# Optimization experiments

Measured on AMD Instinct MI355X. Metric: run time of the kernel, lower is better.

Reference implementation:

```python
import jax, jax.numpy as jnp
import numpy as np

# ---- model hyperparams (match init_kwargs / Mamba1 defaults) ----
SEQ_LEN, PRED_LEN, PATCH, STRIDE = 512, 96, 16, 16
D_MODEL, N_LAYER, N_VARS = 128, 2, 32
D_INNER, D_STATE, D_CONV, DT_RANK = 2 * D_MODEL, 16, 4, 8  # d_inner=2*d_model, dt_rank=ceil(d_model/16)
BATCH = 16
EPS = 1e-5


def setup_inputs() -> dict:
    key = jax.random.key(0)
    ks = jax.random.split(key, 20)
    s = 0.02
    inp = {
        'x_enc': jax.random.normal(ks[0], (BATCH, SEQ_LEN, N_VARS), jnp.float32),
        'x_mark_enc': jax.random.normal(ks[1], (BATCH, SEQ_LEN, 4), jnp.float32),
        'x_dec': jax.random.normal(ks[2], (BATCH, PRED_LEN, N_VARS), jnp.float32),
        'x_mark_dec': jax.random.normal(ks[3], (BATCH, PRED_LEN, 4), jnp.float32),
        # patch embedding: Linear(patch_len -> d_model, bias=False)
        'patch_w': jax.random.normal(ks[4], (D_MODEL, PATCH), jnp.float32) * s,
        # per-layer Mamba1 params, stacked on leading layer axis
        'norm_w': jnp.ones((N_LAYER, D_MODEL), jnp.float32),
        'in_proj_w': jax.random.normal(ks[5], (N_LAYER, 2 * D_INNER, D_MODEL), jnp.float32) * s,
        'conv_w': jax.random.normal(ks[6], (N_LAYER, D_INNER, D_CONV), jnp.float32) * s,
        'conv_b': jnp.zeros((N_LAYER, D_INNER), jnp.float32),
        'x_proj_w': jax.random.normal(ks[7], (N_LAYER, DT_RANK + 2 * D_STATE, D_INNER), jnp.float32) * s,
        'dt_proj_w': jax.random.normal(ks[8], (N_LAYER, D_INNER, DT_RANK), jnp.float32) * s,
        'dt_proj_b': jax.random.normal(ks[9], (N_LAYER, D_INNER), jnp.float32) * 0.1 - 4.0,  # softplus -> small dt
        'A_log': jnp.tile(jnp.log(jnp.arange(1, D_STATE + 1, dtype=jnp.float32))[None, None, :], (N_LAYER, D_INNER, 1)),
        'D_skip': jnp.ones((N_LAYER, D_INNER), jnp.float32),
        'out_proj_w': jax.random.normal(ks[10], (N_LAYER, D_MODEL, D_INNER), jnp.float32) * s,
        'final_norm_w': jnp.ones((D_MODEL,), jnp.float32),
        # head: Linear(d_model*seq_len//patch_len -> pred_len)
        'head_w': jax.random.normal(ks[11], (PRED_LEN, D_MODEL * SEQ_LEN // PATCH), jnp.float32) * s,
        'head_b': jnp.zeros((PRED_LEN,), jnp.float32),
    }
    return inp


def rmsnorm(x, w):
    return x * jax.lax.rsqrt(jnp.mean(x * x, axis=-1, keepdims=True) + EPS) * w


def selective_scan(u, dt, A, Bm, Cm, Dp):
    # u, dt: (B,L,Di); Bm, Cm: (B,L,N); A: (Di,N); Dp: (Di,)
    def step(h, inp):
        dt_t, B_t, C_t, u_t = inp  # (B,Di),(B,N),(B,N),(B,Di)
        dA = jnp.exp(dt_t[:, :, None] * A)                      # (B,Di,N)
        h = dA * h + dt_t[:, :, None] * B_t[:, None, :] * u_t[:, :, None]
        y = jnp.einsum('bdn,bn->bd', h, C_t)
        return h, y

    B_, L, Di = u.shape
    h0 = jnp.zeros((B_, Di, A.shape[1]), u.dtype)
    xs = (dt.transpose(1, 0, 2), Bm.transpose(1, 0, 2), Cm.transpose(1, 0, 2), u.transpose(1, 0, 2))
    _, ys = jax.lax.scan(step, h0, xs)
    return ys.transpose(1, 0, 2) + u * Dp  # skip connection D*u


def mamba_mixer(x, in_w, cw, cb, xp_w, dt_w, dt_b, A_log, Dp, out_w):
    # x: (B,L,d_model)
    xz = x @ in_w.T                                   # (B,L,2*Di)
    xs_, z = jnp.split(xz, 2, axis=-1)
    xc = xs_.transpose(0, 2, 1)                       # (B,Di,L)
    xc = jax.lax.conv_general_dilated(
        xc, cw[:, None, :], (1,), [(D_CONV - 1, 0)],  # causal depthwise conv
        dimension_numbers=('NCH', 'OIH', 'NCH'), feature_group_count=D_INNER)
    xc = jax.nn.silu(xc + cb[None, :, None])
    u = xc.transpose(0, 2, 1)                         # (B,L,Di)
    x_dbl = u @ xp_w.T                                # (B,L,dt_rank+2N)
    dt, Bm, Cm = jnp.split(x_dbl, [DT_RANK, DT_RANK + D_STATE], axis=-1)
    dt = jax.nn.softplus(dt @ dt_w.T + dt_b)          # (B,L,Di)
    A = -jnp.exp(A_log)                               # (Di,N)
    y = selective_scan(u, dt, A, Bm, Cm, Dp)
    y = y * jax.nn.silu(z)
    return y @ out_w.T


def reference(x_enc, x_mark_enc, x_dec, x_mark_dec, patch_w, norm_w, in_proj_w,
              conv_w, conv_b, x_proj_w, dt_proj_w, dt_proj_b, A_log, D_skip,
              out_proj_w, final_norm_w, head_w, head_b):
    b, _, c = x_enc.shape
    # instance norm over time (stats detached)
    means = jax.lax.stop_gradient(jnp.mean(x_enc, axis=1, keepdims=True))
    xe = x_enc - means
    stdev = jax.lax.stop_gradient(jnp.sqrt(jnp.var(xe, axis=1, keepdims=True) + EPS))
    xe = xe / stdev
    # patching: stride == patch_len so unfold == reshape
    xp = xe.transpose(0, 2, 1).reshape(b, c, SEQ_LEN // PATCH, PATCH)  # (b,c,l,patch)
    enc = jnp.einsum('bclp,dp->bcld', xp, patch_w).reshape(b, c * (SEQ_LEN // PATCH), D_MODEL)
    # Mamba encoder: pre-norm residual blocks + final norm
    x = enc
    for i in range(N_LAYER):
        h = rmsnorm(x, norm_w[i])
        x = x + mamba_mixer(h, in_proj_w[i], conv_w[i], conv_b[i], x_proj_w[i],
                            dt_proj_w[i], dt_proj_b[i], A_log[i], D_skip[i], out_proj_w[i])
    x = rmsnorm(x, final_norm_w)
    # prediction head: b (c l) d -> (b c) (l d) -> linear -> (b, pred, c)
    l = SEQ_LEN // PATCH
    xh = x.reshape(b, c, l * D_MODEL)
    out = xh @ head_w.T + head_b                      # (b,c,pred)
    dec_out = out.transpose(0, 2, 1)                  # (b,pred,c)
    dec_out = dec_out * stdev[:, :1, :] + means[:, :1, :]
    return dec_out
```

## Files before the change

kernel.cpp:

```cpp
#include <hip/hip_runtime.h>
#include <hip/hip_bf16.h>
#include <math.h>

#define BATCH   16
#define SEQL    512
#define NVARS   32
#define PATCHL  16
#define LTOK    32
#define DMODEL  128
#define NLAYER  2
#define DIN     256
#define DSTATE  16
#define DTRANK  8
#define DCONV   4
#define PRED    96
#define TOK     1024
#define NTOK    (BATCH*TOK)
#define EPSF    1e-5f
#define NCH     64
#define CHL     16

typedef __attribute__((ext_vector_type(8))) short bf16x8;
typedef __attribute__((ext_vector_type(4))) float f32x4;
typedef __hip_bfloat16 bf16;

__global__ __launch_bounds__(256) void k_cast(
    const float* __restrict__ a, const float* __restrict__ b,
    const float* __restrict__ c, const float* __restrict__ d,
    int na, int nb, int nc, int nd, bf16* __restrict__ out,
    const float* __restrict__ A_log, float* __restrict__ a1s, int* __restrict__ pwf,
    float* __restrict__ hg)
{
    int i = blockIdx.x * 256 + threadIdx.x;
    int total = na + nb + nc + nd;
    if (i < total) {
        float v;
        if (i < na) v = a[i];
        else if (i < na + nb) v = b[i - na];
        else if (i < na + nb + nc) v = c[i - na - nb];
        else v = d[i - na - nb - nc];
        out[i] = __float2bfloat16(v);
    } else if (i < total + NLAYER * DIN) {
        int j = i - total;
        const float* al = A_log + (size_t)j * DSTATE;
        float a1 = -__expf(al[0]);
        bool pw = true;
        #pragma unroll
        for (int n = 1; n < 16; n++) {
            float av = -__expf(al[n]);
            pw = pw && (fabsf(av - (n + 1) * a1) <= 1e-5f * fabsf((n + 1) * a1));
        }
        a1s[j] = a1;
        pwf[j] = pw ? 1 : 0;
    } else if (i < total + NLAYER * DIN + 512 * PRED) {
        hg[i - total - NLAYER * DIN] = 0.f;
    }
}

__global__ __launch_bounds__(256) void k_instnorm_patch(
    const float* __restrict__ x_enc, const float* __restrict__ patch_w,
    const float* __restrict__ nw0,
    float* __restrict__ x, bf16* __restrict__ hbf,
    float* __restrict__ means, float* __restrict__ stdev)
{
    int bc = blockIdx.x;
    int b = bc >> 5, c = bc & 31;
    __shared__ float xe[SEQL];
    __shared__ float pw[DMODEL * PATCHL];
    __shared__ float red[8];
    __shared__ float enc_lds[LTOK][DMODEL];
    int tid = threadIdx.x;

    float v0 = x_enc[((size_t)b * SEQL + tid) * NVARS + c];
    float v1 = x_enc[((size_t)b * SEQL + tid + 256) * NVARS + c];
    for (int i = tid; i < DMODEL * PATCHL; i += 256) pw[i] = patch_w[i];

    float s = v0 + v1;
    for (int o = 1; o < 64; o <<= 1) s += __shfl_xor(s, o, 64);
    if ((tid & 63) == 0) red[tid >> 6] = s;
    __syncthreads();
    float mean = (red[0] + red[1] + red[2] + red[3]) * (1.f / 512.f);

    float d0 = v0 - mean, d1 = v1 - mean;
    float q = d0 * d0 + d1 * d1;
    for (int o = 1; o < 64; o <<= 1) q += __shfl_xor(q, o, 64);
    if ((tid & 63) == 0) red[4 + (tid >> 6)] = q;
    __syncthreads();
    float var = (red[4] + red[5] + red[6] + red[7]) * (1.f / 512.f);
    float sd = sqrtf(var + EPSF);
    float rsd = 1.f / sd;
    if (tid == 0) { means[bc] = mean; stdev[bc] = sd; }

    xe[tid] = d0 * rsd;
    xe[tid + 256] = d1 * rsd;
    __syncthreads();

    size_t base = ((size_t)b * TOK + (size_t)c * LTOK) * DMODEL;
    for (int o = tid; o < LTOK * DMODEL; o += 256) {
        int l = o >> 7, dm = o & 127;
        float acc = 0.f;
        #pragma unroll
        for (int p = 0; p < PATCHL; p++) acc += xe[l * PATCHL + p] * pw[dm * PATCHL + p];
        x[base + o] = acc;
        enc_lds[l][dm] = acc;
    }
    __syncthreads();

    int t = tid >> 3, g = tid & 7;
    float vals[16];
    float ss = 0.f;
    #pragma unroll
    for (int j = 0; j < 16; j++) { vals[j] = enc_lds[t][g * 16 + j]; ss += vals[j] * vals[j]; }
    ss += __shfl_xor(ss, 1, 64);
    ss += __shfl_xor(ss, 2, 64);
    ss += __shfl_xor(ss, 4, 64);
    float rms = rsqrtf(ss * (1.f / DMODEL) + EPSF);
    bf16* hp = hbf + (base + (size_t)t * DMODEL);
    #pragma unroll
    for (int j = 0; j < 16; j++)
        hp[g * 16 + j] = __float2bfloat16(vals[j] * rms * nw0[g * 16 + j]);
}

__global__ __launch_bounds__(256) void mfma_gemm_at(
    const bf16* __restrict__ A, const bf16* __restrict__ W,
    float* __restrict__ C, int M, int N, int K, int kper)
{
    __shared__ ushort Asm[128][40];
    __shared__ ushort Wsm[128][40];
    int bm = blockIdx.y * 128, bn = blockIdx.x * 128;
    int tid = threadIdx.x;
    int w = tid >> 6, l = tid & 63;
    int wr = w >> 1, wc = w & 1;
    int kb = (l >> 4) * 8, lr = l & 15;

    f32x4 acc[4][4];
    #pragma unroll
    for (int i = 0; i < 4; i++)
        #pragma unroll
        for (int j = 0; j < 4; j++) acc[i][j] = (f32x4){0.f, 0.f, 0.f, 0.f};

    int kbeg = blockIdx.z * kper;
    for (int k0 = kbeg; k0 < kbeg + kper; k0 += 32) {
        #pragma unroll
        for (int i = 0; i < 2; i++) {
            int idx = tid + 256 * i;
            int row = idx >> 2, kq = (idx & 3) * 8;
            *(float4*)&Asm[row][kq] =
                *(const float4*)&A[(size_t)(bm + row) * K + k0 + kq];
            float4 wv = make_float4(0.f, 0.f, 0.f, 0.f);
            if (bn + row < N)
                wv = *(const float4*)&W[(size_t)(bn + row) * K + k0 + kq];
            *(float4*)&Wsm[row][kq] = wv;
        }
        __syncthreads();
        bf16x8 af[4], bfr[4];
        #pragma unroll
        for (int f = 0; f < 4; f++) {
            af[f]  = *(const bf16x8*)&Asm[wr * 64 + f * 16 + lr][kb];
            bfr[f] = *(const bf16x8*)&Wsm[wc * 64 + f * 16 + lr][kb];
        }
        #pragma unroll
        for (int mf = 0; mf < 4; mf++)
            #pragma unroll
            for (int nf = 0; nf < 4; nf++)
                acc[mf][nf] = __builtin_amdgcn_mfma_f32_16x16x32_bf16(
                    af[mf], bfr[nf], acc[mf][nf], 0, 0, 0);
        __syncthreads();
    }

    int rbase = bm + wr * 64 + (l >> 4) * 4;
    int cbase = bn + wc * 64 + lr;
    #pragma unroll
    for (int mf = 0; mf < 4; mf++) {
        #pragma unroll
        for (int nf = 0; nf < 4; nf++) {
            int n = cbase + nf * 16;
            if (n >= N) continue;
            #pragma unroll
            for (int r = 0; r < 4; r++)
                atomicAdd(&C[(size_t)(rbase + mf * 16 + r) * N + n], acc[mf][nf][r]);
        }
    }
}

__device__ __forceinline__ float softplus_f(float x) {
    return (x > 8.f) ? x : __logf(1.f + __expf(x));
}

__global__ __launch_bounds__(256) void k_convx1(
    const bf16* __restrict__ hbf, const bf16* __restrict__ iwA,
    const float* __restrict__ cw, const float* __restrict__ cb,
    const bf16* __restrict__ xw,
    const float* __restrict__ dtw, const float* __restrict__ dtb_,
    const float* __restrict__ a1s, const int* __restrict__ pwf,
    const float* __restrict__ A_log,
    bf16* __restrict__ ubf, float* __restrict__ xdbl,
    bf16* __restrict__ q, float* __restrict__ sdt_out)
{
    int blk = blockIdx.x;
    int b = blk >> 6, ch = blk & (NCH - 1);
    int d = threadIdx.x;
    __shared__ ushort hb_lds[32][136];
    __shared__ ushort xs_lds[32][264];
    __shared__ ushort u_lds[16][264];
    __shared__ float xdbl_lds[16][40];

    int tloc0 = ch * CHL;

    {
        int r = d >> 3, c8 = (d & 7) * 16;
        int tl = tloc0 - 16 + r;
        float4 v0 = make_float4(0.f, 0.f, 0.f, 0.f), v1 = v0;
        if (tl >= 0) {
            const bf16* src = hbf + ((size_t)b * TOK + tl) * DMODEL + c8;
            v0 = *(const float4*)src;
            v1 = *(const float4*)(src + 8);
        }
        *(float4*)&hb_lds[r][c8] = v0;
        *(float4*)&hb_lds[r][c8 + 8] = v1;
    }
    __syncthreads();

    {
        int w = d >> 6, l = d & 63;
        int lr = l & 15, kb = (l >> 4) * 8;
        f32x4 accx[2][4];
        #pragma unroll
        for (int mf = 0; mf < 2; mf++)
            #pragma unroll
            for (int nf = 0; nf < 4; nf++) accx[mf][nf] = (f32x4){0.f, 0.f, 0.f, 0.f};
        #pragma unroll
        for (int ks = 0; ks < 4; ks++) {
            bf16x8 af0 = *(const bf16x8*)&hb_lds[lr][ks * 32 + kb];
            bf16x8 af1 = *(const bf16x8*)&hb_lds[16 + lr][ks * 32 + kb];
            #pragma unroll
            for (int nf = 0; nf < 4; nf++) {
                const bf16* wrow = iwA + (size_t)(w * 64 + nf * 16 + lr) * DMODEL;
                bf16x8 bfr = *(const bf16x8*)&wrow[ks * 32 + kb];
                accx[0][nf] = __builtin_amdgcn_mfma_f32_16x16x32_bf16(af0, bfr, accx[0][nf], 0, 0, 0);
                accx[1][nf] = __builtin_amdgcn_mfma_f32_16x16x32_bf16(af1, bfr, accx[1][nf], 0, 0, 0);
            }
        }
        #pragma unroll
        for (int mf = 0; mf < 2; mf++)
            #pragma unroll
            for (int nf = 0; nf < 4; nf++) {
                int ncol = w * 64 + nf * 16 + lr;
                #pragma unroll
                for (int r = 0; r < 4; r++) {
                    int row = mf * 16 + (l >> 4) * 4 + r;
                    bf16 xb = __float2bfloat16(accx[mf][nf][r]);
                    xs_lds[row][ncol] = *(ushort*)&xb;
                }
            }
    }
    __syncthreads();

    float c0 = cw[d * 4], c1 = cw[d * 4 + 1], c2 = cw[d * 4 + 2], c3 = cw[d * 4 + 3];
    float cbias = cb[d];
    float xv[19];
    #pragma unroll
    for (int i = 0; i < 19; i++) {
        ushort raw = xs_lds[13 + i][d];
        xv[i] = __bfloat162float(*(bf16*)&raw);
    }
    bf16* uout = ubf + ((size_t)b * TOK + tloc0) * 256 + d;
    #pragma unroll
    for (int t = 0; t < 16; t++) {
        float a = cbias + xv[t] * c0 + xv[t + 1] * c1 + xv[t + 2] * c2 + xv[t + 3] * c3;
        float s = __fdividef(a, 1.f + __expf(-a));
        bf16 ub = __float2bfloat16(s);
        u_lds[t][d] = *(ushort*)&ub;
        uout[(size_t)t * 256] = ub;
    }
    __syncthreads();

    {
        int w = d >> 6, l = d & 63;
        if (w < 3) {
            int lr = l & 15, kb = (l >> 4) * 8;
            int nrow = w * 16 + lr;
            bool valid = nrow < 40;
            const bf16* wrow = xw + (size_t)nrow * 256;
            f32x4 acc = (f32x4){0.f, 0.f, 0.f, 0.f};
            #pragma unroll
            for (int ks = 0; ks < 8; ks++) {
                bf16x8 af = *(const bf16x8*)&u_lds[lr][ks * 32 + kb];
                bf16x8 bfr = (bf16x8){0, 0, 0, 0, 0, 0, 0, 0};
                if (valid) bfr = *(const bf16x8*)&wrow[ks * 32 + kb];
                acc = __builtin_amdgcn_mfma_f32_16x16x32_bf16(af, bfr, acc, 0, 0, 0);
            }
            int ncol = w * 16 + (l & 15);
            if (ncol < 40) {
                #pragma unroll
                for (int r = 0; r < 4; r++) {
                    int t = (l >> 4) * 4 + r;
                    xdbl_lds[t][ncol] = acc[r];
                    xdbl[((size_t)b * TOK + tloc0 + t) * 40 + ncol] = acc[r];
                }
            }
        }
    }
    __syncthreads();

    float a1 = a1s[d];
    bool pw = pwf[d] != 0;
    float w8[8];
    #pragma unroll
    for (int j = 0; j < 8; j++) w8[j] = dtw[d * 8 + j];
    float bias = dtb_[d];
    float h[16];
    #pragma unroll
    for (int n = 0; n < 16; n++) h[n] = 0.f;
    float sdt = 0.f;

    if (pw) {
        for (int t = 0; t < CHL; t++) {
            float acc = bias;
            #pragma unroll
            for (int j = 0; j < 8; j++) acc += xdbl_lds[t][j] * w8[j];
            float dtv = softplus_f(acc);
            ushort uraw = u_lds[t][d];
            float uu = __bfloat162float(*(bf16*)&uraw);
            sdt += dtv;
            float du = dtv * uu;
            float dA[16];
            dA[0] = __expf(dtv * a1);
            #pragma unroll
            for (int n = 1; n < 16; n++) dA[n] = dA[(n - 1) >> 1] * dA[n >> 1];
            #pragma unroll
            for (int n = 0; n < 16; n++)
                h[n] = dA[n] * h[n] + du * xdbl_lds[t][8 + n];
        }
    } else {
        float Av[16];
        #pragma unroll
        for (int n = 0; n < 16; n++) Av[n] = -__expf(A_log[d * 16 + n]);
        for (int t = 0; t < CHL; t++) {
            float acc = bias;
            #pragma unroll
            for (int j = 0; j < 8; j++) acc += xdbl_lds[t][j] * w8[j];
            float dtv = softplus_f(acc);
            ushort uraw = u_lds[t][d];
            float uu = __bfloat162float(*(bf16*)&uraw);
            sdt += dtv;
            float du = dtv * uu;
            #pragma unroll
            for (int n = 0; n < 16; n++)
                h[n] = __expf(dtv * Av[n]) * h[n] + du * xdbl_lds[t][8 + n];
        }
    }
    bf16* qp = q + ((size_t)blk * 16) * 256 + d;
    #pragma unroll
    for (int n = 0; n < 16; n++) qp[(size_t)n * 256] = __float2bfloat16(h[n]);
    sdt_out[(size_t)blk * 256 + d] = sdt;
}

__global__ __launch_bounds__(256) void k_scan2(
    const float* __restrict__ A_log, const float* __restrict__ sdt_in,
    bf16* __restrict__ q)
{
    int idx = blockIdx.x * 256 + threadIdx.x;
    int d = idx & 255, n = (idx >> 8) & 15, b = idx >> 12;
    float Av = -__expf(A_log[d * 16 + n]);
    float h = 0.f;
    for (int g = 0; g < NCH / 8; g++) {
        float qv[8], sv[8];
        #pragma unroll
        for (int j = 0; j < 8; j++) {
            size_t blk = (size_t)b * NCH + g * 8 + j;
            qv[j] = __bfloat162float(q[(blk * 16 + n) * 256 + d]);
            sv[j] = sdt_in[blk * 256 + d];
        }
        #pragma unroll
        for (int j = 0; j < 8; j++) {
            size_t blk = (size_t)b * NCH + g * 8 + j;
            float P = __expf(Av * sv[j]);
            q[(blk * 16 + n) * 256 + d] = __float2bfloat16(h);
            h = P * h + qv[j];
        }
    }
}

__global__ __launch_bounds__(256) void k_scan3o(
    const bf16* __restrict__ ubf, const float* __restrict__ xdbl,
    const bf16* __restrict__ iwZ,
    const float* __restrict__ dtw, const float* __restrict__ dtb_,
    const float* __restrict__ a1s, const int* __restrict__ pwf,
    const float* __restrict__ A_log, const float* __restrict__ Dp,
    const bf16* __restrict__ q, const bf16* __restrict__ ow,
    const float* __restrict__ nwn,
    float* __restrict__ x, bf16* __restrict__ hbf)
{
    int blk = blockIdx.x;
    int b = blk >> 6, ch = blk & (NCH - 1);
    int d = threadIdx.x;
    __shared__ ushort hz_lds[16][136];
    __shared__ ushort z_lds[16][264];
    __shared__ ushort y_lds[16][264];
    __shared__ float xn_lds[16][132];

    size_t tok0 = (size_t)b * TOK + ch * CHL;

    {
        int r = d >> 4, c8 = (d & 15) * 8;
        *(float4*)&hz_lds[r][c8] = *(const float4*)(hbf + (tok0 + r) * DMODEL + c8);
    }
    __syncthreads();

    {
        int w = d >> 6, l = d & 63;
        int lr = l & 15, kb = (l >> 4) * 8;
        f32x4 accz[4];
        #pragma unroll
        for (int nf = 0; nf < 4; nf++) accz[nf] = (f32x4){0.f, 0.f, 0.f, 0.f};
        #pragma unroll
        for (int ks = 0; ks < 4; ks++) {
            bf16x8 af = *(const bf16x8*)&hz_lds[lr][ks * 32 + kb];
            #pragma unroll
            for (int nf = 0; nf < 4; nf++) {
                const bf16* wrow = iwZ + (size_t)(w * 64 + nf * 16 + lr) * DMODEL;
                bf16x8 bfr = *(const bf16x8*)&wrow[ks * 32 + kb];
                accz[nf] = __builtin_amdgcn_mfma_f32_16x16x32_bf16(af, bfr, accz[nf], 0, 0, 0);
            }
        }
        #pragma unroll
        for (int nf = 0; nf < 4; nf++) {
            int ncol = w * 64 + nf * 16 + lr;
            #pragma unroll
            for (int r = 0; r < 4; r++) {
                bf16 zb = __float2bfloat16(accz[nf][r]);
                z_lds[(l >> 4) * 4 + r][ncol] = *(ushort*)&zb;
            }
        }
    }
    __syncthreads();

    float a1 = a1s[d];
    bool pw = pwf[d] != 0;
    float w8[8];
    #pragma unroll
    for (int j = 0; j < 8; j++) w8[j] = dtw[d * 8 + j];
    float bias = dtb_[d];
    float Dv = Dp[d];
    float h[16];
    const bf16* qp = q + ((size_t)blk * 16) * 256 + d;
    #pragma unroll
    for (int n = 0; n < 16; n++) h[n] = __bfloat162float(qp[(size_t)n * 256]);

    const float* row = xdbl + tok0 * 40;
    const bf16* up = ubf + tok0 * 256 + d;

    if (pw) {
        for (int t = 0; t < CHL; t++, row += 40, up += 256) {
            float acc = bias;
            #pragma unroll
            for (int j = 0; j < 8; j++) acc += row[j] * w8[j];
            float dtv = softplus_f(acc);
            float uu = __bfloat162float(*up);
            float du = dtv * uu;
            float dA[16];
            dA[0] = __expf(dtv * a1);
            #pragma unroll
            for (int n = 1; n < 16; n++) dA[n] = dA[(n - 1) >> 1] * dA[n >> 1];
            float ya = 0.f;
            #pragma unroll
            for (int n = 0; n < 16; n++) {
                h[n] = dA[n] * h[n] + du * row[8 + n];
                ya += h[n] * row[24 + n];
            }
            ushort zraw = z_lds[t][d];
            float zv = __bfloat162float(*(bf16*)&zraw);
            float sz = __fdividef(zv, 1.f + __expf(-zv));
            bf16 yb = __float2bfloat16((ya + uu * Dv) * sz);
            y_lds[t][d] = *(ushort*)&yb;
        }
    } else {
        float Av[16];
        #pragma unroll
        for (int n = 0; n < 16; n++) Av[n] = -__expf(A_log[d * 16 + n]);
        for (int t = 0; t < CHL; t++, row += 40, up += 256) {
            float acc = bias;
            #pragma unroll
            for (int j = 0; j < 8; j++) acc += row[j] * w8[j];
            float dtv = softplus_f(acc);
            float uu = __bfloat162float(*up);
            float du = dtv * uu;
            float ya = 0.f;
            #pragma unroll
            for (int n = 0; n < 16; n++) {
                h[n] = __expf(dtv * Av[n]) * h[n] + du * row[8 + n];
                ya += h[n] * row[24 + n];
            }
            ushort zraw = z_lds[t][d];
            float zv = __bfloat162float(*(bf16*)&zraw);
            float sz = __fdividef(zv, 1.f + __expf(-zv));
            bf16 yb = __float2bfloat16((ya + uu * Dv) * sz);
            y_lds[t][d] = *(ushort*)&yb;
        }
    }
    __syncthreads();

    int w = d >> 6, l = d & 63;
    int lr = l & 15, kb = (l >> 4) * 8;
    const bf16* wr0 = ow + (size_t)(w * 32 + lr) * 256;
    const bf16* wr1 = ow + (size_t)(w * 32 + 16 + lr) * 256;
    f32x4 acc0 = (f32x4){0.f, 0.f, 0.f, 0.f};
    f32x4 acc1 = (f32x4){0.f, 0.f, 0.f, 0.f};
    #pragma unroll
    for (int ks = 0; ks < 8; ks++) {
        bf16x8 af = *(const bf16x8*)&y_lds[lr][ks * 32 + kb];
        bf16x8 b0 = *(const bf16x8*)&wr0[ks * 32 + kb];
        bf16x8 b1 = *(const bf16x8*)&wr1[ks * 32 + kb];
        acc0 = __builtin_amdgcn_mfma_f32_16x16x32_bf16(af, b0, acc0, 0, 0, 0);
        acc1 = __builtin_amdgcn_mfma_f32_16x16x32_bf16(af, b1, acc1, 0, 0, 0);
    }
    int trow = (l >> 4) * 4;
    float* xp = x + (tok0 + trow) * (size_t)DMODEL;
    #pragma unroll
    for (int r = 0; r < 4; r++) {
        float v0 = xp[(size_t)r * DMODEL + w * 32 + lr] + acc0[r];
        float v1 = xp[(size_t)r * DMODEL + w * 32 + 16 + lr] + acc1[r];
        xp[(size_t)r * DMODEL + w * 32 + lr] = v0;
        xp[(size_t)r * DMODEL + w * 32 + 16 + lr] = v1;
        xn_lds[trow + r][w * 32 + lr] = v0;
        xn_lds[trow + r][w * 32 + 16 + lr] = v1;
    }
    __syncthreads();

    int t = d >> 4, g = d & 15;
    float vals[8];
    float ss = 0.f;
    #pragma unroll
    for (int j = 0; j < 8; j++) { vals[j] = xn_lds[t][g * 8 + j]; ss += vals[j] * vals[j]; }
    ss += __shfl_xor(ss, 1, 64);
    ss += __shfl_xor(ss, 2, 64);
    ss += __shfl_xor(ss, 4, 64);
    ss += __shfl_xor(ss, 8, 64);
    float rms = rsqrtf(ss * (1.f / DMODEL) + EPSF);
    bf16* hp = hbf + (tok0 + t) * (size_t)DMODEL;
    #pragma unroll
    for (int j = 0; j < 8; j++)
        hp[g * 8 + j] = __float2bfloat16(vals[j] * rms * nwn[g * 8 + j]);
}

__global__ __launch_bounds__(256) void k_head_ep(
    const float* __restrict__ hg, const float* __restrict__ hb,
    const float* __restrict__ means, const float* __restrict__ stdev,
    float* __restrict__ out)
{
    int i = blockIdx.x * 256 + threadIdx.x;
    if (i >= BATCH * PRED * NVARS) return;
    int c = i & 31;
    int p = (i >> 5) % PRED;
    int b = i / (PRED * NVARS);
    float v = hg[((size_t)b * NVARS + c) * PRED + p] + hb[p];
    out[i] = v * stdev[b * NVARS + c] + means[b * NVARS + c];
}

extern "C" void kernel_launch(void* const* d_in, const int* in_sizes, int n_in,
                              void* d_out, int out_size, void* d_ws, size_t ws_size,
                              hipStream_t stream)
{
    const float* x_enc   = (const float*)d_in[0];
    const float* patch_w = (const float*)d_in[4];
    const float* norm_w  = (const float*)d_in[5];
    const float* in_w    = (const float*)d_in[6];
    const float* conv_w  = (const float*)d_in[7];
    const float* conv_b  = (const float*)d_in[8];
    const float* xp_w    = (const float*)d_in[9];
    const float* dt_w    = (const float*)d_in[10];
    const float* dt_b    = (const float*)d_in[11];
    const float* A_log   = (const float*)d_in[12];
    const float* D_skip  = (const float*)d_in[13];
    const float* out_w   = (const float*)d_in[14];
    const float* fnorm_w = (const float*)d_in[15];
    const float* head_w  = (const float*)d_in[16];
    const float* head_b  = (const float*)d_in[17];
    float* out = (float*)d_out;

    float* ws    = (float*)d_ws;
    float* means = ws;
    float* stdv  = ws + 512;
    float* x     = ws + 1024;
    float* xdbl  = x    + (size_t)NTOK * 128;
    float* sbuf  = xdbl + (size_t)NTOK * 40;
    float* hg    = sbuf + (size_t)BATCH * NCH * DIN;
    float* a1s   = hg + 512 * PRED;
    int*   pwf   = (int*)(a1s + NLAYER * DIN);
    bf16* hbf  = (bf16*)(pwf + NLAYER * DIN);
    bf16* ubf  = hbf + (size_t)NTOK * 128;
    bf16* qbuf = ubf + (size_t)NTOK * 256;
    bf16* wbf  = qbuf + (size_t)BATCH * NCH * DSTATE * DIN;

    const int NIW = NLAYER * 2 * DIN * DMODEL;
    const int NXW = NLAYER * (DTRANK + 2*DSTATE) * DIN;
    const int NOW = NLAYER * DMODEL * DIN;
    const int NHW = PRED * LTOK * DMODEL;
    bf16* iwbf = wbf;
    bf16* xwbf = iwbf + NIW;
    bf16* owbf = xwbf + NXW;
    bf16* hwbf = owbf + NOW;

    int castN = NIW + NXW + NOW + NHW + NLAYER * DIN + 512 * PRED;
    k_cast<<<(castN + 255) / 256, 256, 0, stream>>>(
        in_w, xp_w, out_w, head_w, NIW, NXW, NOW, NHW, wbf, A_log, a1s, pwf, hg);

    k_instnorm_patch<<<BATCH * NVARS, 256, 0, stream>>>(
        x_enc, patch_w, norm_w, x, hbf, means, stdv);

    for (int layer = 0; layer < NLAYER; layer++) {
        const float* cw  = conv_w + layer * DIN * DCONV;
        const float* cb  = conv_b + layer * DIN;
        const float* dw  = dt_w   + layer * DIN * DTRANK;
        const float* db  = dt_b   + layer * DIN;
        const float* al  = A_log  + layer * DIN * DSTATE;
        const float* dp  = D_skip + layer * DIN;
        const float* a1l = a1s + layer * DIN;
        const int*   pwl = pwf + layer * DIN;
        const bf16* iwA = iwbf + (size_t)layer * 2 * DIN * DMODEL;
        const bf16* iwZ = iwA + (size_t)DIN * DMODEL;
        const bf16* xw = xwbf + (size_t)layer * (DTRANK + 2 * DSTATE) * DIN;
        const bf16* ow = owbf + (size_t)layer * DMODEL * DIN;
        const float* nwn = (layer + 1 < NLAYER) ? (norm_w + (layer + 1) * DMODEL) : fnorm_w;

        k_convx1<<<BATCH * NCH, 256, 0, stream>>>(
            hbf, iwA, cw, cb, xw, dw, db, a1l, pwl, al, ubf, xdbl, qbuf, sbuf);
        k_scan2<<<(BATCH * DIN * DSTATE) / 256, 256, 0, stream>>>(al, sbuf, qbuf);
        k_scan3o<<<BATCH * NCH, 256, 0, stream>>>(
            ubf, xdbl, iwZ, dw, db, a1l, pwl, al, dp, qbuf, ow, nwn, x, hbf);
    }

    mfma_gemm_at<<<dim3(1, 4, 32), 256, 0, stream>>>(
        hbf, hwbf, hg, 512, PRED, LTOK * DMODEL, 128);
    k_head_ep<<<(BATCH * PRED * NVARS + 255) / 256, 256, 0, stream>>>(
        hg, head_b, means, stdv, out);
}
```

Before: 155.0 us.

## Merge cast and instnorm kernels; pass packed u and dt to scan pass

The weight-cast/A-precompute kernel and the instance-norm/patch-embedding kernel are merged into one launch that uses extra blocks for the cast work, which saves one launch. The first scan kernel now stores u and the softplus dt packed as two bf16 values in one 32-bit word. The second scan kernel then reads dt directly instead of recomputing the dt projection and softplus per token. This trades an extra 2 bytes per element of write and read traffic for less recomputation, and it rounds dt to bf16, which may slightly change accuracy.

Result: no change. 152.2 us (-1.8%).

```diff
diff --git a/kernel.cpp b/kernel.cpp
--- a/kernel.cpp
+++ b/kernel.cpp
@@ -20,56 +20,66 @@
 #define NCH     64
 #define CHL     16
 
+#define NIW (NLAYER * 2 * DIN * DMODEL)
+#define NXW (NLAYER * (DTRANK + 2*DSTATE) * DIN)
+#define NOW (NLAYER * DMODEL * DIN)
+#define NHW (PRED * LTOK * DMODEL)
+#define TOTW (NIW + NXW + NOW + NHW)
+
 typedef __attribute__((ext_vector_type(8))) short bf16x8;
 typedef __attribute__((ext_vector_type(4))) float f32x4;
 typedef __hip_bfloat16 bf16;
 
-__global__ __launch_bounds__(256) void k_cast(
-    const float* __restrict__ a, const float* __restrict__ b,
-    const float* __restrict__ c, const float* __restrict__ d,
-    int na, int nb, int nc, int nd, bf16* __restrict__ out,
-    const float* __restrict__ A_log, float* __restrict__ a1s, int* __restrict__ pwf,
+__device__ __forceinline__ float softplus_f(float x) {
+    return (x > 8.f) ? x : __logf(1.f + __expf(x));
+}
+
+__global__ __launch_bounds__(256) void k_init(
+    const float* __restrict__ x_enc, const float* __restrict__ patch_w,
+    const float* __restrict__ nw0,
+    const float* __restrict__ in_w, const float* __restrict__ xp_w,
+    const float* __restrict__ out_w, const float* __restrict__ head_w,
+    const float* __restrict__ A_log,
+    float* __restrict__ x, bf16* __restrict__ hbf,
+    float* __restrict__ means, float* __restrict__ stdev,
+    bf16* __restrict__ wbf, float* __restrict__ a1s, int* __restrict__ pwf,
     float* __restrict__ hg)
 {
-    int i = blockIdx.x * 256 + threadIdx.x;
-    int total = na + nb + nc + nd;
-    if (i < total) {
-        float v;
-        if (i < na) v = a[i];
-        else if (i < na + nb) v = b[i - na];
-        else if (i < na + nb + nc) v = c[i - na - nb];
-        else v = d[i - na - nb - nc];
-        out[i] = __float2bfloat16(v);
-    } else if (i < total + NLAYER * DIN) {
-        int j = i - total;
-        const float* al = A_log + (size_t)j * DSTATE;
-        float a1 = -__expf(al[0]);
-        bool pw = true;
-        #pragma unroll
-        for (int n = 1; n < 16; n++) {
-            float av = -__expf(al[n]);
-            pw = pw && (fabsf(av - (n + 1) * a1) <= 1e-5f * fabsf((n + 1) * a1));
-        }
-        a1s[j] = a1;
-        pwf[j] = pw ? 1 : 0;
-    } else if (i < total + NLAYER * DIN + 512 * PRED) {
-        hg[i - total - NLAYER * DIN] = 0.f;
-    }
-}
-
-__global__ __launch_bounds__(256) void k_instnorm_patch(
-    const float* __restrict__ x_enc, const float* __restrict__ patch_w,
-    const float* __restrict__ nw0,
-    float* __restrict__ x, bf16* __restrict__ hbf,
-    float* __restrict__ means, float* __restrict__ stdev)
-{
-    int bc = blockIdx.x;
-    int b = bc >> 5, c = bc & 31;
     __shared__ float xe[SEQL];
     __shared__ float pw[DMODEL * PATCHL];
     __shared__ float red[8];
     __shared__ float enc_lds[LTOK][DMODEL];
     int tid = threadIdx.x;
+
+    if (blockIdx.x >= BATCH * NVARS) {
+        int i = (blockIdx.x - BATCH * NVARS) * 256 + tid;
+        if (i < TOTW) {
+            float v;
+            if (i < NIW) v = in_w[i];
+            else if (i < NIW + NXW) v = xp_w[i - NIW];
+            else if (i < NIW + NXW + NOW) v = out_w[i - NIW - NXW];
+            else v = head_w[i - NIW - NXW - NOW];
+            wbf[i] = __float2bfloat16(v);
+        } else if (i < TOTW + NLAYER * DIN) {
+            int j = i - TOTW;
+            const float* al = A_log + (size_t)j * DSTATE;
+            float a1 = -__expf(al[0]);
+            bool pwok = true;
+            #pragma unroll
+            for (int n = 1; n < 16; n++) {
+                float av = -__expf(al[n]);
+                pwok = pwok && (fabsf(av - (n + 1) * a1) <= 1e-5f * fabsf((n + 1) * a1));
+            }
+            a1s[j] = a1;
+            pwf[j] = pwok ? 1 : 0;
+        } else if (i < TOTW + NLAYER * DIN + 512 * PRED) {
+            hg[i - TOTW - NLAYER * DIN] = 0.f;
+        }
+        return;
+    }
+
+    int bc = blockIdx.x;
+    int b = bc >> 5, c = bc & 31;
 
     float v0 = x_enc[((size_t)b * SEQL + tid) * NVARS + c];
     float v1 = x_enc[((size_t)b * SEQL + tid + 256) * NVARS + c];
@@ -183,10 +193,6 @@
     }
 }
 
-__device__ __forceinline__ float softplus_f(float x) {
-    return (x > 8.f) ? x : __logf(1.f + __expf(x));
-}
-
 __global__ __launch_bounds__(256) void k_convx1(
     const bf16* __restrict__ hbf, const bf16* __restrict__ iwA,
     const float* __restrict__ cw, const float* __restrict__ cb,
@@ -194,7 +200,7 @@
     const float* __restrict__ dtw, const float* __restrict__ dtb_,
     const float* __restrict__ a1s, const int* __restrict__ pwf,
     const float* __restrict__ A_log,
-    bf16* __restrict__ ubf, float* __restrict__ xdbl,
+    unsigned int* __restrict__ udb, float* __restrict__ xdbl,
     bf16* __restrict__ q, float* __restrict__ sdt_out)
 {
     int blk = blockIdx.x;
@@ -256,22 +262,22 @@
     }
     __syncthreads();
 
-    float c0 = cw[d * 4], c1 = cw[d * 4 + 1], c2 = cw[d * 4 + 2], c3 = cw[d * 4 + 3];
-    float cbias = cb[d];
-    float xv[19];
-    #pragma unroll
-    for (int i = 0; i < 19; i++) {
-        ushort raw = xs_lds[13 + i][d];
-        xv[i] = __bfloat162float(*(bf16*)&raw);
-    }
-    bf16* uout = ubf + ((size_t)b * TOK + tloc0) * 256 + d;
-    #pragma unroll
-    for (int t = 0; t < 16; t++) {
-        float a = cbias + xv[t] * c0 + xv[t + 1] * c1 + xv[t + 2] * c2 + xv[t + 3] * c3;
-        float s = __fdividef(a, 1.f + __expf(-a));
-        bf16 ub = __float2bfloat16(s);
-        u_lds[t][d] = *(ushort*)&ub;
-        uout[(size_t)t * 256] = ub;
+    {
+        float c0 = cw[d * 4], c1 = cw[d * 4 + 1], c2 = cw[d * 4 + 2], c3 = cw[d * 4 + 3];
+        float cbias = cb[d];
+        float xv[19];
+        #pragma unroll
+        for (int i = 0; i < 19; i++) {
+            ushort raw = xs_lds[13 + i][d];
+            xv[i] = __bfloat162float(*(bf16*)&raw);
+        }
+        #pragma unroll
+        for (int t = 0; t < 16; t++) {
+            float a = cbias + xv[t] * c0 + xv[t + 1] * c1 + xv[t + 2] * c2 + xv[t + 3] * c3;
+            float s = __fdividef(a, 1.f + __expf(-a));
+            bf16 ub = __float2bfloat16(s);
+            u_lds[t][d] = *(ushort*)&ub;
+        }
     }
     __syncthreads();
 
@@ -313,6 +319,7 @@
     #pragma unroll
     for (int n = 0; n < 16; n++) h[n] = 0.f;
     float sdt = 0.f;
+    unsigned int* udp = udb + ((size_t)b * TOK + tloc0) * 256 + d;
 
     if (pw) {
         for (int t = 0; t < CHL; t++) {
@@ -331,6 +338,8 @@
             #pragma unroll
             for (int n = 0; n < 16; n++)
                 h[n] = dA[n] * h[n] + du * xdbl_lds[t][8 + n];
+            bf16 dv = __float2bfloat16(dtv);
+            udp[(size_t)t * 256] = (unsigned int)uraw | ((unsigned int)(*(ushort*)&dv) << 16);
         }
     } else {
         float Av[16];
@@ -348,6 +357,8 @@
             #pragma unroll
             for (int n = 0; n < 16; n++)
                 h[n] = __expf(dtv * Av[n]) * h[n] + du * xdbl_lds[t][8 + n];
+            bf16 dv = __float2bfloat16(dtv);
+            udp[(size_t)t * 256] = (unsigned int)uraw | ((unsigned int)(*(ushort*)&dv) << 16);
         }
     }
     bf16* qp = q + ((size_t)blk * 16) * 256 + d;
@@ -383,9 +394,8 @@
 }
 
 __global__ __launch_bounds__(256) void k_scan3o(
-    const bf16* __restrict__ ubf, const float* __restrict__ xdbl,
+    const unsigned int* __restrict__ udb, const float* __restrict__ xdbl,
     const bf16* __restrict__ iwZ,
-    const float* __restrict__ dtw, const float* __restrict__ dtb_,
     const float* __restrict__ a1s, const int* __restrict__ pwf,
     const float* __restrict__ A_log, const float* __restrict__ Dp,
     const bf16* __restrict__ q, const bf16* __restrict__ ow,
@@ -438,10 +448,6 @@
 
     float a1 = a1s[d];
     bool pw = pwf[d] != 0;
-    float w8[8];
-    #pragma unroll
-    for (int j = 0; j < 8; j++) w8[j] = dtw[d * 8 + j];
-    float bias = dtb_[d];
     float Dv = Dp[d];
     float h[16];
     const bf16* qp = q + ((size_t)blk * 16) * 256 + d;
@@ -449,15 +455,14 @@
     for (int n = 0; n < 16; n++) h[n] = __bfloat162float(qp[(size_t)n * 256]);
 
     const float* row = xdbl + tok0 * 40;
-    const bf16* up = ubf + tok0 * 256 + d;
+    const unsigned int* up = udb + tok0 * 256 + d;
 
     if (pw) {
         for (int t = 0; t < CHL; t++, row += 40, up += 256) {
-            float acc = bias;
-            #pragma unroll
-            for (int j = 0; j < 8; j++) acc += row[j] * w8[j];
-            float dtv = softplus_f(acc);
-            float uu = __bfloat162float(*up);
+            unsigned int ud = *up;
+            ushort ulo = (ushort)(ud & 0xffffu), dhi = (ushort)(ud >> 16);
+            float uu = __bfloat162float(*(bf16*)&ulo);
+            float dtv = __bfloat162float(*(bf16*)&dhi);
             float du = dtv * uu;
             float dA[16];
             dA[0] = __expf(dtv * a1);
@@ -480,11 +485,10 @@
         #pragma unroll
         for (int n = 0; n < 16; n++) Av[n] = -__expf(A_log[d * 16 + n]);
         for (int t = 0; t < CHL; t++, row += 40, up += 256) {
-            float acc = bias;
-            #pragma unroll
-            for (int j = 0; j < 8; j++) acc += row[j] * w8[j];
-            float dtv = softplus_f(acc);
-            float uu = __bfloat162float(*up);
+            unsigned int ud = *up;
+            ushort ulo = (ushort)(ud & 0xffffu), dhi = (ushort)(ud >> 16);
+            float uu = __bfloat162float(*(bf16*)&ulo);
+            float dtv = __bfloat162float(*(bf16*)&dhi);
             float du = dtv * uu;
             float ya = 0.f;
             #pragma unroll
@@ -528,20 +532,22 @@
     }
     __syncthreads();
 
-    int t = d >> 4, g = d & 15;
-    float vals[8];
-    float ss = 0.f;
-    #pragma unroll
-    for (int j = 0; j < 8; j++) { vals[j] = xn_lds[t][g * 8 + j]; ss += vals[j] * vals[j]; }
-    ss += __shfl_xor(ss, 1, 64);
-    ss += __shfl_xor(ss, 2, 64);
-    ss += __shfl_xor(ss, 4, 64);
-    ss += __shfl_xor(ss, 8, 64);
-    float rms = rsqrtf(ss * (1.f / DMODEL) + EPSF);
-    bf16* hp = hbf + (tok0 + t) * (size_t)DMODEL;
-    #pragma unroll
-    for (int j = 0; j < 8; j++)
-        hp[g * 8 + j] = __float2bfloat16(vals[j] * rms * nwn[g * 8 + j]);
+    {
+        int t = d >> 4, g = d & 15;
+        float vals[8];
+        float ss = 0.f;
+        #pragma unroll
+        for (int j = 0; j < 8; j++) { vals[j] = xn_lds[t][g * 8 + j]; ss += vals[j] * vals[j]; }
+        ss += __shfl_xor(ss, 1, 64);
+        ss += __shfl_xor(ss, 2, 64);
+        ss += __shfl_xor(ss, 4, 64);
+        ss += __shfl_xor(ss, 8, 64);
+        float rms = rsqrtf(ss * (1.f / DMODEL) + EPSF);
+        bf16* hp = hbf + (tok0 + t) * (size_t)DMODEL;
+        #pragma unroll
+        for (int j = 0; j < 8; j++)
+            hp[g * 8 + j] = __float2bfloat16(vals[j] * rms * nwn[g * 8 + j]);
+    }
 }
 
 __global__ __launch_bounds__(256) void k_head_ep(
@@ -588,26 +594,21 @@
     float* hg    = sbuf + (size_t)BATCH * NCH * DIN;
     float* a1s   = hg + 512 * PRED;
     int*   pwf   = (int*)(a1s + NLAYER * DIN);
-    bf16* hbf  = (bf16*)(pwf + NLAYER * DIN);
-    bf16* ubf  = hbf + (size_t)NTOK * 128;
-    bf16* qbuf = ubf + (size_t)NTOK * 256;
+    unsigned int* udb = (unsigned int*)(pwf + NLAYER * DIN);
+    bf16* hbf  = (bf16*)(udb + (size_t)NTOK * 256);
+    bf16* qbuf = hbf + (size_t)NTOK * 128;
     bf16* wbf  = qbuf + (size_t)BATCH * NCH * DSTATE * DIN;
 
-    const int NIW = NLAYER * 2 * DIN * DMODEL;
-    const int NXW = NLAYER * (DTRANK + 2*DSTATE) * DIN;
-    const int NOW = NLAYER * DMODEL * DIN;
-    const int NHW = PRED * LTOK * DMODEL;
     bf16* iwbf = wbf;
     bf16* xwbf = iwbf + NIW;
     bf16* owbf = xwbf + NXW;
     bf16* hwbf = owbf + NOW;
 
-    int castN = NIW + NXW + NOW + NHW + NLAYER * DIN + 512 * PRED;
-    k_cast<<<(castN + 255) / 256, 256, 0, stream>>>(
-        in_w, xp_w, out_w, head_w, NIW, NXW, NOW, NHW, wbf, A_log, a1s, pwf, hg);
-
-    k_instnorm_patch<<<BATCH * NVARS, 256, 0, stream>>>(
-        x_enc, patch_w, norm_w, x, hbf, means, stdv);
+    int castN = TOTW + NLAYER * DIN + 512 * PRED;
+    int initBlocks = BATCH * NVARS + (castN + 255) / 256;
+    k_init<<<initBlocks, 256, 0, stream>>>(
+        x_enc, patch_w, norm_w, in_w, xp_w, out_w, head_w, A_log,
+        x, hbf, means, stdv, wbf, a1s, pwf, hg);
 
     for (int layer = 0; layer < NLAYER; layer++) {
         const float* cw  = conv_w + layer * DIN * DCONV;
@@ -625,10 +626,10 @@
         const float* nwn = (layer + 1 < NLAYER) ? (norm_w + (layer + 1) * DMODEL) : fnorm_w;
 
         k_convx1<<<BATCH * NCH, 256, 0, stream>>>(
-            hbf, iwA, cw, cb, xw, dw, db, a1l, pwl, al, ubf, xdbl, qbuf, sbuf);
+            hbf, iwA, cw, cb, xw, dw, db, a1l, pwl, al, udb, xdbl, qbuf, sbuf);
         k_scan2<<<(BATCH * DIN * DSTATE) / 256, 256, 0, stream>>>(al, sbuf, qbuf);
         k_scan3o<<<BATCH * NCH, 256, 0, stream>>>(
-            ubf, xdbl, iwZ, dw, db, a1l, pwl, al, dp, qbuf, ow, nwn, x, hbf);
+            udb, xdbl, iwZ, a1l, pwl, al, dp, qbuf, ow, nwn, x, hbf);
     }
 
     mfma_gemm_at<<<dim3(1, 4, 32), 256, 0, stream>>>(
```
